# Optimization experiments

Hardware: AMD Instinct MI355X
Metric: run time of the kernel (lower is better)

Reference implementation:

```python
import jax, jax.numpy as jnp
import numpy as np


def setup_inputs() -> dict:
    key = jax.random.key(0)
    N, M, D = 4, 8192, 64
    x = jax.random.normal(key, (N, M, D), dtype=jnp.float32)
    return {"x": x, "k": 16}


def reference(x, k):
    """KNNGraph forward (algorithm='bruteforce-blas', dist='euclidean',
    exclude_self=False). Returns (src, dst) edge arrays: for each node j in
    point set i (global id i*M + j), its k nearest neighbors (including
    itself) are edge sources, the node is the destination."""
    N, M, D = x.shape
    # Squared euclidean pairwise distances via BLAS: |a|^2 + |b|^2 - 2 a.b
    x2 = jnp.sum(x * x, axis=-1)                       # (N, M)
    dots = jnp.einsum('nmd,npd->nmp', x, x)            # (N, M, M)
    d2 = x2[:, :, None] + x2[:, None, :] - 2.0 * dots  # (N, M, M)
    # k smallest distances per row -> top_k on negated distances
    _, idx = jax.lax.top_k(-d2, k)                     # (N, M, k) neighbor ids
    offset = (jnp.arange(N, dtype=idx.dtype) * M)[:, None, None]
    src = (idx + offset).reshape(-1)                   # (N*M*k,)
    dst = jnp.repeat(jnp.arange(N * M, dtype=idx.dtype), k)
    return src, dst
```

## Files before the change

### kernel.cpp

```cpp
#include <hip/hip_runtime.h>


#define MM 8192
#define NN 4
#define DD 64
#define KK 16
#define TK 20
#define TILE 64
#define NROWS (NN * MM)
#define FB 10

typedef float f32x2 __attribute__((ext_vector_type(2)));

__global__ __launch_bounds__(256) void norms_np_kernel(
    const float* __restrict__ x, float* __restrict__ x2) {
#pragma clang fp contract(off)
  int r = blockIdx.x * 256 + threadIdx.x;
  if (r >= NROWS) return;
  const float4* p = (const float4*)(x + (size_t)r * DD);
  float s[DD];
#pragma unroll
  for (int i = 0; i < DD / 4; ++i) {
    float4 v = p[i];
    s[4 * i + 0] = v.x * v.x;
    s[4 * i + 1] = v.y * v.y;
    s[4 * i + 2] = v.z * v.z;
    s[4 * i + 3] = v.w * v.w;
  }
  float acc[4][4];
#pragma unroll
  for (int c = 0; c < 4; ++c)
#pragma unroll
    for (int l = 0; l < 4; ++l) acc[c][l] = s[4 * c + l];
#pragma unroll
  for (int b = 1; b < 4; ++b)
#pragma unroll
    for (int c = 0; c < 4; ++c)
#pragma unroll
      for (int l = 0; l < 4; ++l)
        acc[c][l] = acc[c][l] + s[16 * b + 4 * c + l];
  float S[4];
#pragma unroll
  for (int l = 0; l < 4; ++l)
    S[l] = (acc[0][l] + acc[1][l]) + (acc[2][l] + acc[3][l]);
  x2[r] = (S[0] + S[1]) + (S[2] + S[3]);
}

#define PSTEP(sA, sB)                       \
  do {                                      \
    unsigned lo_ = min((sA), (sB));         \
    unsigned hi_ = max((sA), (sB));         \
    (sA) = lo_; (sB) = hi_;                 \
  } while (0)

#define PBUBBLE20(S)                                              \
  do {                                                            \
    PSTEP(S##18, S##19); PSTEP(S##17, S##18); PSTEP(S##16, S##17);\
    PSTEP(S##15, S##16); PSTEP(S##14, S##15); PSTEP(S##13, S##14);\
    PSTEP(S##12, S##13); PSTEP(S##11, S##12); PSTEP(S##10, S##11);\
    PSTEP(S##9,  S##10); PSTEP(S##8,  S##9);  PSTEP(S##7,  S##8); \
    PSTEP(S##6,  S##7);  PSTEP(S##5,  S##6);  PSTEP(S##4,  S##5); \
    PSTEP(S##3,  S##4);  PSTEP(S##2,  S##3);  PSTEP(S##1,  S##2); \
    PSTEP(S##0,  S##1);                                           \
  } while (0)

#define PDECL20(S)                                                          \
  unsigned S##0 = 0xFFFFFFFFu, S##1 = 0xFFFFFFFFu, S##2 = 0xFFFFFFFFu,      \
           S##3 = 0xFFFFFFFFu, S##4 = 0xFFFFFFFFu, S##5 = 0xFFFFFFFFu,      \
           S##6 = 0xFFFFFFFFu, S##7 = 0xFFFFFFFFu, S##8 = 0xFFFFFFFFu,      \
           S##9 = 0xFFFFFFFFu, S##10 = 0xFFFFFFFFu, S##11 = 0xFFFFFFFFu,    \
           S##12 = 0xFFFFFFFFu, S##13 = 0xFFFFFFFFu, S##14 = 0xFFFFFFFFu,   \
           S##15 = 0xFFFFFFFFu, S##16 = 0xFFFFFFFFu, S##17 = 0xFFFFFFFFu,   \
           S##18 = 0xFFFFFFFFu, S##19 = 0xFFFFFFFFu;

#define PSTORE20RAW(BASE, S)                                                \
  do {                                                                      \
    pi[(BASE) + 0]  = (int)S##0;  pi[(BASE) + 1]  = (int)S##1;              \
    pi[(BASE) + 2]  = (int)S##2;  pi[(BASE) + 3]  = (int)S##3;              \
    pi[(BASE) + 4]  = (int)S##4;  pi[(BASE) + 5]  = (int)S##5;              \
    pi[(BASE) + 6]  = (int)S##6;  pi[(BASE) + 7]  = (int)S##7;              \
    pi[(BASE) + 8]  = (int)S##8;  pi[(BASE) + 9]  = (int)S##9;              \
    pi[(BASE) + 10] = (int)S##10; pi[(BASE) + 11] = (int)S##11;             \
    pi[(BASE) + 12] = (int)S##12; pi[(BASE) + 13] = (int)S##13;             \
    pi[(BASE) + 14] = (int)S##14; pi[(BASE) + 15] = (int)S##15;             \
    pi[(BASE) + 16] = (int)S##16; pi[(BASE) + 17] = (int)S##17;             \
    pi[(BASE) + 18] = (int)S##18; pi[(BASE) + 19] = (int)S##19;             \
  } while (0)

#define PSTORE20(BASE, S, C0)                                               \
  do {                                                                      \
    pi[(BASE) + 0]  = (int)(S##0  & IMASK) + (C0);                          \
    pi[(BASE) + 1]  = (int)(S##1  & IMASK) + (C0);                          \
    pi[(BASE) + 2]  = (int)(S##2  & IMASK) + (C0);                          \
    pi[(BASE) + 3]  = (int)(S##3  & IMASK) + (C0);                          \
    pi[(BASE) + 4]  = (int)(S##4  & IMASK) + (C0);                          \
    pi[(BASE) + 5]  = (int)(S##5  & IMASK) + (C0);                          \
    pi[(BASE) + 6]  = (int)(S##6  & IMASK) + (C0);                          \
    pi[(BASE) + 7]  = (int)(S##7  & IMASK) + (C0);                          \
    pi[(BASE) + 8]  = (int)(S##8  & IMASK) + (C0);                          \
    pi[(BASE) + 9]  = (int)(S##9  & IMASK) + (C0);                          \
    pi[(BASE) + 10] = (int)(S##10 & IMASK) + (C0);                          \
    pi[(BASE) + 11] = (int)(S##11 & IMASK) + (C0);                          \
    pi[(BASE) + 12] = (int)(S##12 & IMASK) + (C0);                          \
    pi[(BASE) + 13] = (int)(S##13 & IMASK) + (C0);                          \
    pi[(BASE) + 14] = (int)(S##14 & IMASK) + (C0);                          \
    pi[(BASE) + 15] = (int)(S##15 & IMASK) + (C0);                          \
    pi[(BASE) + 16] = (int)(S##16 & IMASK) + (C0);                          \
    pi[(BASE) + 17] = (int)(S##17 & IMASK) + (C0);                          \
    pi[(BASE) + 18] = (int)(S##18 & IMASK) + (C0);                          \
    pi[(BASE) + 19] = (int)(S##19 & IMASK) + (C0);                          \
  } while (0)

#define PK2(QF4, WLO, WHI, ACC0, ACC1)                             \
  do {                                                             \
    f32x2 qlo_ = {(QF4).x, (QF4).y};                               \
    f32x2 qhi_ = {(QF4).z, (QF4).w};                               \
    ACC0 = __builtin_elementwise_fma(qlo_, (WLO), ACC0);           \
    ACC1 = __builtin_elementwise_fma(qhi_, (WHI), ACC1);           \
  } while (0)

template <int P>
__global__ __launch_bounds__(256)
__attribute__((amdgpu_waves_per_eu(2, 4)))
void knn_partial2_kernel(
    const float* __restrict__ x, const float* __restrict__ x2,
    int* __restrict__ pi) {
  constexpr int IB = (P == 16) ? 9 : (P == 8) ? 10 : (P == 4) ? 11 : 12;
  constexpr unsigned IMASK = (1u << IB) - 1u;
  constexpr unsigned QMASK = ~IMASK;

  __shared__ unsigned lbufA[FB * 256];
  __shared__ unsigned lbufB[FB * 256];

  const int tid      = threadIdx.x;
  const int rb       = blockIdx.x / P;
  const int chunk    = blockIdx.x % P;
  const int base_row = rb * 512;
  const int b        = base_row >> 13;
  const int rowA     = base_row + tid;
  const int rowB     = rowA + 256;
  const int jA       = rowA & (MM - 1);
  const int jB       = jA + 256;

  const float* __restrict__ xb  = x + (size_t)b * MM * DD;
  const float* __restrict__ x2b = x2 + b * MM;

  const float4* qpA = (const float4*)(xb + (size_t)jA * DD);
  const float4* qpB = (const float4*)(xb + (size_t)jB * DD);
  float4 qa0 = qpA[0],  qa1 = qpA[1],  qa2 = qpA[2],  qa3 = qpA[3];
  float4 qa4 = qpA[4],  qa5 = qpA[5],  qa6 = qpA[6],  qa7 = qpA[7];
  float4 qa8 = qpA[8],  qa9 = qpA[9],  qa10 = qpA[10], qa11 = qpA[11];
  float4 qa12 = qpA[12], qa13 = qpA[13], qa14 = qpA[14], qa15 = qpA[15];
  float4 qb0 = qpB[0],  qb1 = qpB[1],  qb2 = qpB[2],  qb3 = qpB[3];
  float4 qb4 = qpB[4],  qb5 = qpB[5],  qb6 = qpB[6],  qb7 = qpB[7];
  float4 qb8 = qpB[8],  qb9 = qpB[9],  qb10 = qpB[10], qb11 = qpB[11];
  float4 qb12 = qpB[12], qb13 = qpB[13], qb14 = qpB[14], qb15 = qpB[15];

  PDECL20(sa)
  PDECL20(sb)
  int cA = 0, cB = 0;

#define FLUSHQ()                                                   \
  do {                                                             \
    _Pragma("unroll")                                              \
    for (int t_ = 0; t_ < FB; ++t_) {                              \
      if (t_ < cA) {                                               \
        unsigned pk_ = lbufA[t_ * 256 + tid];                      \
        sa19 = min(sa19, pk_);                                     \
        PBUBBLE20(sa);                                             \
      }                                                            \
      if (t_ < cB) {                                               \
        unsigned pk_ = lbufB[t_ * 256 + tid];                      \
        sb19 = min(sb19, pk_);                                     \
        PBUBBLE20(sb);                                             \
      }                                                            \
    }                                                              \
    cA = 0;                                                        \
    cB = 0;                                                        \
  } while (0)

  const int C  = MM / P;
  const int c0 = chunk * C;

#pragma unroll 1
  for (int c = c0; c < c0 + C; c += 2) {
    const float4* cp0 = (const float4*)(xb + (size_t)c * DD);
    const float4* cp1 = (const float4*)(xb + (size_t)(c + 1) * DD);
    float x2c0 = x2b[c];
    float x2c1 = x2b[c + 1];

    float4 u0 = cp0[0],  u1 = cp0[1],  u2 = cp0[2],  u3 = cp0[3];
    float4 u4 = cp0[4],  u5 = cp0[5],  u6 = cp0[6],  u7 = cp0[7];
    float4 u8 = cp0[8],  u9 = cp0[9],  u10 = cp0[10], u11 = cp0[11];
    float4 u12 = cp0[12], u13 = cp0[13], u14 = cp0[14], u15 = cp0[15];
    float4 t0 = cp1[0],  t1 = cp1[1],  t2 = cp1[2],  t3 = cp1[3];
    float4 t4 = cp1[4],  t5 = cp1[5],  t6 = cp1[6],  t7 = cp1[7];
    float4 t8 = cp1[8],  t9 = cp1[9],  t10 = cp1[10], t11 = cp1[11];
    float4 t12 = cp1[12], t13 = cp1[13], t14 = cp1[14], t15 = cp1[15];

    {
      f32x2 aA0 = {0.f, 0.f}, aA1 = {0.f, 0.f};
      f32x2 aB0 = {0.f, 0.f}, aB1 = {0.f, 0.f};
      {
        f32x2 wlo, whi;
#define USEW(W)  wlo = (f32x2){(W).x, (W).y}; whi = (f32x2){(W).z, (W).w}
        USEW(u0);  PK2(qa0,  wlo, whi, aA0, aA1); PK2(qb0,  wlo, whi, aB0, aB1);
        USEW(u1);  PK2(qa1,  wlo, whi, aA0, aA1); PK2(qb1,  wlo, whi, aB0, aB1);
        USEW(u2);  PK2(qa2,  wlo, whi, aA0, aA1); PK2(qb2,  wlo, whi, aB0, aB1);
        USEW(u3);  PK2(qa3,  wlo, whi, aA0, aA1); PK2(qb3,  wlo, whi, aB0, aB1);
        USEW(u4);  PK2(qa4,  wlo, whi, aA0, aA1); PK2(qb4,  wlo, whi, aB0, aB1);
        USEW(u5);  PK2(qa5,  wlo, whi, aA0, aA1); PK2(qb5,  wlo, whi, aB0, aB1);
        USEW(u6);  PK2(qa6,  wlo, whi, aA0, aA1); PK2(qb6,  wlo, whi, aB0, aB1);
        USEW(u7);  PK2(qa7,  wlo, whi, aA0, aA1); PK2(qb7,  wlo, whi, aB0, aB1);
        USEW(u8);  PK2(qa8,  wlo, whi, aA0, aA1); PK2(qb8,  wlo, whi, aB0, aB1);
        USEW(u9);  PK2(qa9,  wlo, whi, aA0, aA1); PK2(qb9,  wlo, whi, aB0, aB1);
        USEW(u10); PK2(qa10, wlo, whi, aA0, aA1); PK2(qb10, wlo, whi, aB0, aB1);
        USEW(u11); PK2(qa11, wlo, whi, aA0, aA1); PK2(qb11, wlo, whi, aB0, aB1);
        USEW(u12); PK2(qa12, wlo, whi, aA0, aA1); PK2(qb12, wlo, whi, aB0, aB1);
        USEW(u13); PK2(qa13, wlo, whi, aA0, aA1); PK2(qb13, wlo, whi, aB0, aB1);
        USEW(u14); PK2(qa14, wlo, whi, aA0, aA1); PK2(qb14, wlo, whi, aB0, aB1);
        USEW(u15); PK2(qa15, wlo, whi, aA0, aA1); PK2(qb15, wlo, whi, aB0, aB1);
      }
      f32x2 rA = aA0 + aA1;
      f32x2 rB = aB0 + aB1;
      float dotA = rA.x + rA.y;
      float dotB = rB.x + rB.y;
      float keyA = fmaf(-2.f, dotA, x2c0);
      float keyB = fmaf(-2.f, dotB, x2c0);

      int kiA = __float_as_int(keyA);
      unsigned monoA = (unsigned)kiA ^ ((unsigned)(kiA >> 31) | 0x80000000u);
      unsigned pkA = (monoA & QMASK) | (unsigned)(c - c0);
      if (pkA < sa19) { lbufA[cA * 256 + tid] = pkA; ++cA; }

      int kiB = __float_as_int(keyB);
      unsigned monoB = (unsigned)kiB ^ ((unsigned)(kiB >> 31) | 0x80000000u);
      unsigned pkB = (monoB & QMASK) | (unsigned)(c - c0);
      if (pkB < sb19) { lbufB[cB * 256 + tid] = pkB; ++cB; }
    }

    {
      f32x2 aA0 = {0.f, 0.f}, aA1 = {0.f, 0.f};
      f32x2 aB0 = {0.f, 0.f}, aB1 = {0.f, 0.f};
      {
        f32x2 wlo, whi;
        USEW(t0);  PK2(qa0,  wlo, whi, aA0, aA1); PK2(qb0,  wlo, whi, aB0, aB1);
        USEW(t1);  PK2(qa1,  wlo, whi, aA0, aA1); PK2(qb1,  wlo, whi, aB0, aB1);
        USEW(t2);  PK2(qa2,  wlo, whi, aA0, aA1); PK2(qb2,  wlo, whi, aB0, aB1);
        USEW(t3);  PK2(qa3,  wlo, whi, aA0, aA1); PK2(qb3,  wlo, whi, aB0, aB1);
        USEW(t4);  PK2(qa4,  wlo, whi, aA0, aA1); PK2(qb4,  wlo, whi, aB0, aB1);
        USEW(t5);  PK2(qa5,  wlo, whi, aA0, aA1); PK2(qb5,  wlo, whi, aB0, aB1);
        USEW(t6);  PK2(qa6,  wlo, whi, aA0, aA1); PK2(qb6,  wlo, whi, aB0, aB1);
        USEW(t7);  PK2(qa7,  wlo, whi, aA0, aA1); PK2(qb7,  wlo, whi, aB0, aB1);
        USEW(t8);  PK2(qa8,  wlo, whi, aA0, aA1); PK2(qb8,  wlo, whi, aB0, aB1);
        USEW(t9);  PK2(qa9,  wlo, whi, aA0, aA1); PK2(qb9,  wlo, whi, aB0, aB1);
        USEW(t10); PK2(qa10, wlo, whi, aA0, aA1); PK2(qb10, wlo, whi, aB0, aB1);
        USEW(t11); PK2(qa11, wlo, whi, aA0, aA1); PK2(qb11, wlo, whi, aB0, aB1);
        USEW(t12); PK2(qa12, wlo, whi, aA0, aA1); PK2(qb12, wlo, whi, aB0, aB1);
        USEW(t13); PK2(qa13, wlo, whi, aA0, aA1); PK2(qb13, wlo, whi, aB0, aB1);
        USEW(t14); PK2(qa14, wlo, whi, aA0, aA1); PK2(qb14, wlo, whi, aB0, aB1);
        USEW(t15); PK2(qa15, wlo, whi, aA0, aA1); PK2(qb15, wlo, whi, aB0, aB1);
#undef USEW
      }
      f32x2 rA = aA0 + aA1;
      f32x2 rB = aB0 + aB1;
      float dotA = rA.x + rA.y;
      float dotB = rB.x + rB.y;
      float keyA = fmaf(-2.f, dotA, x2c1);
      float keyB = fmaf(-2.f, dotB, x2c1);

      int kiA = __float_as_int(keyA);
      unsigned monoA = (unsigned)kiA ^ ((unsigned)(kiA >> 31) | 0x80000000u);
      unsigned pkA = (monoA & QMASK) | (unsigned)(c + 1 - c0);
      if (pkA < sa19) { lbufA[cA * 256 + tid] = pkA; ++cA; }

      int kiB = __float_as_int(keyB);
      unsigned monoB = (unsigned)kiB ^ ((unsigned)(kiB >> 31) | 0x80000000u);
      unsigned pkB = (monoB & QMASK) | (unsigned)(c + 1 - c0);
      if (pkB < sb19) { lbufB[cB * 256 + tid] = pkB; ++cB; }
    }

    if (__any((cA | cB) >= FB - 2)) FLUSHQ();
  }

  FLUSHQ();
#undef FLUSHQ

  size_t baseA = ((size_t)rowA * P + chunk) * TK;
  size_t baseB = ((size_t)rowB * P + chunk) * TK;
  PSTORE20RAW(baseA, sa);
  PSTORE20RAW(baseB, sb);
}

template <int P>
__global__ __launch_bounds__(256)
__attribute__((amdgpu_waves_per_eu(2, 2)))
void knn_partial_q1_kernel(
    const float* __restrict__ x, const float* __restrict__ x2,
    int* __restrict__ pi) {
  constexpr int IB = (P == 8) ? 10 : (P == 4) ? 11 : (P == 2) ? 12 : 13;
  constexpr unsigned IMASK = (1u << IB) - 1u;
  constexpr unsigned QMASK = ~IMASK;

  __shared__ float tile[TILE * DD];
  __shared__ float x2t[TILE];

  const int tid   = threadIdx.x;
  const int rb    = blockIdx.x / P;
  const int chunk = blockIdx.x % P;
  const int b     = rb >> 5;
  const int row   = rb * 256 + tid;
  const int j     = row - b * MM;

  const float* __restrict__ xb  = x + (size_t)b * MM * DD;
  const float* __restrict__ x2b = x2 + b * MM;

  const float4* qp = (const float4*)(xb + (size_t)j * DD);
  float4 q0 = qp[0],  q1 = qp[1],  q2 = qp[2],  q3 = qp[3];
  float4 q4 = qp[4],  q5 = qp[5],  q6 = qp[6],  q7 = qp[7];
  float4 q8 = qp[8],  q9 = qp[9],  q10 = qp[10], q11 = qp[11];
  float4 q12 = qp[12], q13 = qp[13], q14 = qp[14], q15 = qp[15];

  PDECL20(s)

  const int C  = MM / P;
  const int c0 = chunk * C;

  for (int ts = c0; ts < c0 + C; ts += TILE) {
    __syncthreads();
    {
      const float4* gsrc = (const float4*)(xb + (size_t)ts * DD);
      float4* lds4 = (float4*)tile;
#pragma unroll
      for (int u = 0; u < 4; ++u) lds4[tid + 256 * u] = gsrc[tid + 256 * u];
      if (tid < TILE / 4)
        ((float4*)x2t)[tid] = ((const float4*)(x2b + ts))[tid];
    }
    __syncthreads();

#pragma unroll 2
    for (int t = 0; t < TILE; ++t) {
      const float4* cp = (const float4*)(tile + t * DD);
      f32x2 a0 = {0.f, 0.f}, a1 = {0.f, 0.f};
      {
        float4 w;
        f32x2 wlo, whi;
#define LOADW(I)  w = cp[I]; wlo = (f32x2){w.x, w.y}; whi = (f32x2){w.z, w.w}
        LOADW(0);  PK2(q0,  wlo, whi, a0, a1);
        LOADW(1);  PK2(q1,  wlo, whi, a0, a1);
        LOADW(2);  PK2(q2,  wlo, whi, a0, a1);
        LOADW(3);  PK2(q3,  wlo, whi, a0, a1);
        LOADW(4);  PK2(q4,  wlo, whi, a0, a1);
        LOADW(5);  PK2(q5,  wlo, whi, a0, a1);
        LOADW(6);  PK2(q6,  wlo, whi, a0, a1);
        LOADW(7);  PK2(q7,  wlo, whi, a0, a1);
        LOADW(8);  PK2(q8,  wlo, whi, a0, a1);
        LOADW(9);  PK2(q9,  wlo, whi, a0, a1);
        LOADW(10); PK2(q10, wlo, whi, a0, a1);
        LOADW(11); PK2(q11, wlo, whi, a0, a1);
        LOADW(12); PK2(q12, wlo, whi, a0, a1);
        LOADW(13); PK2(q13, wlo, whi, a0, a1);
        LOADW(14); PK2(q14, wlo, whi, a0, a1);
        LOADW(15); PK2(q15, wlo, whi, a0, a1);
#undef LOADW
      }
      f32x2 rr = a0 + a1;
      float dot = rr.x + rr.y;
      float key = fmaf(-2.f, dot, x2t[t]);

      int ki = __float_as_int(key);
      unsigned mono = (unsigned)ki ^ ((unsigned)(ki >> 31) | 0x80000000u);
      unsigned pk = (mono & QMASK) | (unsigned)(ts - c0 + t);
      s19 = min(s19, pk);
      PBUBBLE20(s);
    }
  }

  size_t base = ((size_t)row * P + chunk) * TK;
  PSTORE20(base, s, c0);
}

#define EBLK(QA, QB, QC, QD, W0, W1, W2, W3)                                  \
  do {                                                                        \
    v0 = (QA).x * (W0).x +                                                    \
         ((QB).x * (W1).x + ((QC).x * (W2).x + ((QD).x * (W3).x + v0)));      \
    v1 = (QA).y * (W0).y +                                                    \
         ((QB).y * (W1).y + ((QC).y * (W2).y + ((QD).y * (W3).y + v1)));      \
    v2 = (QA).z * (W0).z +                                                    \
         ((QB).z * (W1).z + ((QC).z * (W2).z + ((QD).z * (W3).z + v2)));      \
    v3 = (QA).w * (W0).w +                                                    \
         ((QB).w * (W1).w + ((QC).w * (W2).w + ((QD).w * (W3).w + v3)));      \
  } while (0)

#define LBSTEP(dA, iA, dB, iB)                                     \
  do {                                                             \
    bool s_ = ((dB) < (dA)) || ((dB) == (dA) && (iB) < (iA));      \
    float tl_ = s_ ? (dB) : (dA);                                  \
    float th_ = s_ ? (dA) : (dB);                                  \
    int   jl_ = s_ ? (iB) : (iA);                                  \
    int   jh_ = s_ ? (iA) : (iB);                                  \
    (dA) = tl_; (dB) = th_; (iA) = jl_; (iB) = jh_;                \
  } while (0)

#define RESCORE_ONE(C_)                                                     \
  {                                                                         \
    int c = (C_);                                                           \
    const float4* pp = (const float4*)(xb + (size_t)c * DD);                \
    float v0 = 0.f, v1 = 0.f, v2 = 0.f, v3 = 0.f;                           \
    {                                                                       \
      float4 w0 = pp[0], w1 = pp[1], w2 = pp[2], w3 = pp[3];                \
      EBLK(q0, q1, q2, q3, w0, w1, w2, w3);                                 \
    }                                                                       \
    {                                                                       \
      float4 w0 = pp[4], w1 = pp[5], w2 = pp[6], w3 = pp[7];                \
      EBLK(q4, q5, q6, q7, w0, w1, w2, w3);                                 \
    }                                                                       \
    {                                                                       \
      float4 w0 = pp[8], w1 = pp[9], w2 = pp[10], w3 = pp[11];              \
      EBLK(q8, q9, q10, q11, w0, w1, w2, w3);                               \
    }                                                                       \
    {                                                                       \
      float4 w0 = pp[12], w1 = pp[13], w2 = pp[14], w3 = pp[15];            \
      EBLK(q12, q13, q14, q15, w0, w1, w2, w3);                             \
    }                                                                       \
    float dotf = (v0 + v1) + (v2 + v3);                                     \
    float s  = x2j + x2[b * MM + c];                                        \
    float tm = 2.0f * dotf;                                                 \
    float d2 = s - tm;                                                      \
    bool lt = (d2 < e15) || (d2 == e15 && c < n15);                         \
    e15 = lt ? d2 : e15;                                                    \
    n15 = lt ? c : n15;                                                     \
    LBSTEP(e14, n14, e15, n15); LBSTEP(e13, n13, e14, n14);                 \
    LBSTEP(e12, n12, e13, n13); LBSTEP(e11, n11, e12, n12);                 \
    LBSTEP(e10, n10, e11, n11); LBSTEP(e9,  n9,  e10, n10);                 \
    LBSTEP(e8,  n8,  e9,  n9);  LBSTEP(e7,  n7,  e8,  n8);                  \
    LBSTEP(e6,  n6,  e7,  n7);  LBSTEP(e5,  n5,  e6,  n6);                  \
    LBSTEP(e4,  n4,  e5,  n5);  LBSTEP(e3,  n3,  e4,  n4);                  \
    LBSTEP(e2,  n2,  e3,  n3);  LBSTEP(e1,  n1,  e2,  n2);                  \
    LBSTEP(e0,  n0,  e1,  n1);                                              \
  }

#define PUBLISH_AND_MERGE8()                                                \
  {                                                                         \
    ls[sub][0][lane]  = make_uint2(MONO(e0),  (unsigned)n0);                \
    ls[sub][1][lane]  = make_uint2(MONO(e1),  (unsigned)n1);                \
    ls[sub][2][lane]  = make_uint2(MONO(e2),  (unsigned)n2);                \
    ls[sub][3][lane]  = make_uint2(MONO(e3),  (unsigned)n3);                \
    ls[sub][4][lane]  = make_uint2(MONO(e4),  (unsigned)n4);                \
    ls[sub][5][lane]  = make_uint2(MONO(e5),  (unsigned)n5);                \
    ls[sub][6][lane]  = make_uint2(MONO(e6),  (unsigned)n6);                \
    ls[sub][7][lane]  = make_uint2(MONO(e7),  (unsigned)n7);                \
    ls[sub][8][lane]  = make_uint2(MONO(e8),  (unsigned)n8);                \
    ls[sub][9][lane]  = make_uint2(MONO(e9),  (unsigned)n9);                \
    ls[sub][10][lane] = make_uint2(MONO(e10), (unsigned)n10);               \
    ls[sub][11][lane] = make_uint2(MONO(e11), (unsigned)n11);               \
    ls[sub][12][lane] = make_uint2(MONO(e12), (unsigned)n12);               \
    ls[sub][13][lane] = make_uint2(MONO(e13), (unsigned)n13);               \
    ls[sub][14][lane] = make_uint2(MONO(e14), (unsigned)n14);               \
    ls[sub][15][lane] = make_uint2(MONO(e15), (unsigned)n15);               \
    __syncthreads();                                                        \
    if (sub == 0) {                                                         \
      uint2 c0v = ls[0][0][lane], c1v = ls[1][0][lane];                     \
      uint2 c2v = ls[2][0][lane], c3v = ls[3][0][lane];                     \
      uint2 c4v = ls[4][0][lane], c5v = ls[5][0][lane];                     \
      uint2 c6v = ls[6][0][lane], c7v = ls[7][0][lane];                     \
      int h0 = 1, h1 = 1, h2 = 1, h3 = 1, h4 = 1, h5 = 1, h6 = 1, h7 = 1;   \
      const uint2 SENT = make_uint2(0xFFFFFFFFu, 0x7FFFFFFFu);              \
      for (int out = 0; out < KK; ++out) {                                  \
        bool l01 = LESS2(c0v, c1v);                                         \
        uint2 m01 = l01 ? c0v : c1v; int w01 = l01 ? 0 : 1;                 \
        bool l23 = LESS2(c2v, c3v);                                         \
        uint2 m23 = l23 ? c2v : c3v; int w23 = l23 ? 2 : 3;                 \
        bool l45 = LESS2(c4v, c5v);                                         \
        uint2 m45 = l45 ? c4v : c5v; int w45 = l45 ? 4 : 5;                 \
        bool l67 = LESS2(c6v, c7v);                                         \
        uint2 m67 = l67 ? c6v : c7v; int w67 = l67 ? 6 : 7;                 \
        bool la = LESS2(m01, m23);                                          \
        uint2 ma = la ? m01 : m23; int wa = la ? w01 : w23;                 \
        bool lb = LESS2(m45, m67);                                          \
        uint2 mb = lb ? m45 : m67; int wb = lb ? w45 : w67;                 \
        bool lf = LESS2(ma, mb);                                            \
        uint2 mv = lf ? ma : mb; int wf = lf ? wa : wb;                     \
        src[(size_t)r * KK + out] = b * MM + (int)mv.y;                     \
        dst[(size_t)r * KK + out] = r;                                      \
        if (wf == 0)      { c0v = (h0 < 16) ? ls[0][h0][lane] : SENT; ++h0; }\
        else if (wf == 1) { c1v = (h1 < 16) ? ls[1][h1][lane] : SENT; ++h1; }\
        else if (wf == 2) { c2v = (h2 < 16) ? ls[2][h2][lane] : SENT; ++h2; }\
        else if (wf == 3) { c3v = (h3 < 16) ? ls[3][h3][lane] : SENT; ++h3; }\
        else if (wf == 4) { c4v = (h4 < 16) ? ls[4][h4][lane] : SENT; ++h4; }\
        else if (wf == 5) { c5v = (h5 < 16) ? ls[5][h5][lane] : SENT; ++h5; }\
        else if (wf == 6) { c6v = (h6 < 16) ? ls[6][h6][lane] : SENT; ++h6; }\
        else              { c7v = (h7 < 16) ? ls[7][h7][lane] : SENT; ++h7; }\
      }                                                                     \
    }                                                                       \
  }

#define MONO(F) ({ int k_ = __float_as_int(F); \
                   (unsigned)k_ ^ ((unsigned)(k_ >> 31) | 0x80000000u); })
#define LESS2(A, B) ((A).x < (B).x || ((A).x == (B).x && (A).y < (B).y))

template <int P>
__global__ __launch_bounds__(256) void knn_rescore8f_kernel(
    const float* __restrict__ x, const float* __restrict__ x2,
    const int* __restrict__ pi,
    int* __restrict__ src, int* __restrict__ dst) {
#pragma clang fp contract(off)
  constexpr int IB = (P == 8) ? 10 : 11;
  constexpr unsigned IMASK = (1u << IB) - 1u;
  constexpr unsigned QMASK = ~IMASK;
  constexpr int CAND = P * TK;
  constexpr int LPT  = CAND / 8;
  constexpr int CC   = MM / P;

  __shared__ unsigned lk[8][LPT][32];
  __shared__ uint2 ls[8][16][32];
  __shared__ unsigned thr[32];

  const int tid  = threadIdx.x;
  const int lane = tid & 31;
  const int sub  = tid >> 5;
  const int r    = blockIdx.x * 32 + lane;
  const int b    = r >> 13;
  const int j    = r & (MM - 1);
  const float* __restrict__ xb = x + (size_t)b * MM * DD;
  const float x2j = x2[r];

  const float4* qp = (const float4*)(xb + (size_t)j * DD);
  float4 q0 = qp[0],  q1 = qp[1],  q2 = qp[2],  q3 = qp[3];
  float4 q4 = qp[4],  q5 = qp[5],  q6 = qp[6],  q7 = qp[7];
  float4 q8 = qp[8],  q9 = qp[9],  q10 = qp[10], q11 = qp[11];
  float4 q12 = qp[12], q13 = qp[13], q14 = qp[14], q15 = qp[15];

  {
    const uint2* pp2 =
        (const uint2*)((const unsigned*)pi + (size_t)r * CAND + sub * LPT);
#pragma unroll
    for (int i = 0; i < LPT / 2; ++i) {
      uint2 v = pp2[i];
      lk[sub][2 * i][lane]     = v.x;
      lk[sub][2 * i + 1][lane] = v.y;
    }
  }
  __syncthreads();

  if (sub == 0) {
    unsigned c0v = lk[0][0][lane], c1v = lk[1][0][lane];
    unsigned c2v = lk[2][0][lane], c3v = lk[3][0][lane];
    unsigned c4v = lk[4][0][lane], c5v = lk[5][0][lane];
    unsigned c6v = lk[6][0][lane], c7v = lk[7][0][lane];
    int h0 = 1, h1 = 1, h2 = 1, h3 = 1, h4 = 1, h5 = 1, h6 = 1, h7 = 1;
    unsigned P16 = 0;
#pragma unroll 1
    for (int out = 0; out < 16; ++out) {
      bool l01 = c0v < c1v; unsigned m01 = l01 ? c0v : c1v; int w01 = l01 ? 0 : 1;
      bool l23 = c2v < c3v; unsigned m23 = l23 ? c2v : c3v; int w23 = l23 ? 2 : 3;
      bool l45 = c4v < c5v; unsigned m45 = l45 ? c4v : c5v; int w45 = l45 ? 4 : 5;
      bool l67 = c6v < c7v; unsigned m67 = l67 ? c6v : c7v; int w67 = l67 ? 6 : 7;
      bool la = m01 < m23; unsigned ma = la ? m01 : m23; int wa = la ? w01 : w23;
      bool lb = m45 < m67; unsigned mb = lb ? m45 : m67; int wb = lb ? w45 : w67;
      bool lf = ma < mb; unsigned mv = lf ? ma : mb; int wf = lf ? wa : wb;
      P16 = mv;
      if (wf == 0)      { c0v = (h0 < LPT) ? lk[0][h0][lane] : 0xFFFFFFFFu; ++h0; }
      else if (wf == 1) { c1v = (h1 < LPT) ? lk[1][h1][lane] : 0xFFFFFFFFu; ++h1; }
      else if (wf == 2) { c2v = (h2 < LPT) ? lk[2][h2][lane] : 0xFFFFFFFFu; ++h2; }
      else if (wf == 3) { c3v = (h3 < LPT) ? lk[3][h3][lane] : 0xFFFFFFFFu; ++h3; }
      else if (wf == 4) { c4v = (h4 < LPT) ? lk[4][h4][lane] : 0xFFFFFFFFu; ++h4; }
      else if (wf == 5) { c5v = (h5 < LPT) ? lk[5][h5][lane] : 0xFFFFFFFFu; ++h5; }
      else if (wf == 6) { c6v = (h6 < LPT) ? lk[6][h6][lane] : 0xFFFFFFFFu; ++h6; }
      else              { c7v = (h7 < LPT) ? lk[7][h7][lane] : 0xFFFFFFFFu; ++h7; }
    }
    thr[lane] = ((P16 & QMASK) + (1u << IB)) | IMASK;
  }
  __syncthreads();
  const unsigned T = thr[lane];

  const float INF = __builtin_inff();
  float e0 = INF, e1 = INF, e2 = INF, e3 = INF, e4 = INF, e5 = INF,
        e6 = INF, e7 = INF, e8 = INF, e9 = INF, e10 = INF, e11 = INF,
        e12 = INF, e13 = INF, e14 = INF, e15 = INF;
  int n0 = 0x7fffffff, n1 = 0x7fffffff, n2 = 0x7fffffff, n3 = 0x7fffffff,
      n4 = 0x7fffffff, n5 = 0x7fffffff, n6 = 0x7fffffff, n7 = 0x7fffffff,
      n8 = 0x7fffffff, n9 = 0x7fffffff, n10 = 0x7fffffff, n11 = 0x7fffffff,
      n12 = 0x7fffffff, n13 = 0x7fffffff, n14 = 0x7fffffff, n15 = 0x7fffffff;

#pragma unroll 1
  for (int t = 0; t < LPT; ++t) {
    unsigned pk = lk[sub][t][lane];
    if (__all((int)(pk > T))) break;
    if (pk <= T) {
      int ent = sub * LPT + t;
      int chunk = ent / TK;
      RESCORE_ONE((int)(pk & IMASK) + chunk * CC)
    }
  }

  PUBLISH_AND_MERGE8()
}

__global__ __launch_bounds__(256) void knn_rescore16f_kernel(
    const float* __restrict__ x, const float* __restrict__ x2,
    const int* __restrict__ pi,
    int* __restrict__ src, int* __restrict__ dst) {
#pragma clang fp contract(off)
  constexpr int IB = 9;
  constexpr unsigned IMASK = (1u << IB) - 1u;
  constexpr unsigned QMASK = ~IMASK;
  constexpr int CAND = 16 * TK;
  constexpr int LPT  = CAND / 8;
  constexpr int CC   = MM / 16;

  __shared__ unsigned lk[16][TK][32];
  __shared__ uint2 ls[8][16][32];
  __shared__ unsigned thr[32];

  const int tid  = threadIdx.x;
  const int lane = tid & 31;
  const int sub  = tid >> 5;
  const int r    = blockIdx.x * 32 + lane;
  const int b    = r >> 13;
  const int j    = r & (MM - 1);
  const float* __restrict__ xb = x + (size_t)b * MM * DD;
  const float x2j = x2[r];

  const float4* qp = (const float4*)(xb + (size_t)j * DD);
  float4 q0 = qp[0],  q1 = qp[1],  q2 = qp[2],  q3 = qp[3];
  float4 q4 = qp[4],  q5 = qp[5],  q6 = qp[6],  q7 = qp[7];
  float4 q8 = qp[8],  q9 = qp[9],  q10 = qp[10], q11 = qp[11];
  float4 q12 = qp[12], q13 = qp[13], q14 = qp[14], q15 = qp[15];

  {
    const uint2* pp2 =
        (const uint2*)((const unsigned*)pi + (size_t)r * CAND + sub * LPT);
#pragma unroll
    for (int i = 0; i < LPT / 2; ++i) {
      int e = sub * LPT + 2 * i;
      uint2 v = pp2[i];
      lk[e / TK][e % TK][lane]       = v.x;
      lk[e / TK][e % TK + 1][lane]   = v.y;
    }
  }
  __syncthreads();

  if (sub == 0) {
    unsigned d0 = lk[0][0][lane],  d1 = lk[1][0][lane];
    unsigned d2 = lk[2][0][lane],  d3 = lk[3][0][lane];
    unsigned d4 = lk[4][0][lane],  d5 = lk[5][0][lane];
    unsigned d6 = lk[6][0][lane],  d7 = lk[7][0][lane];
    unsigned d8 = lk[8][0][lane],  d9 = lk[9][0][lane];
    unsigned d10 = lk[10][0][lane], d11 = lk[11][0][lane];
    unsigned d12 = lk[12][0][lane], d13 = lk[13][0][lane];
    unsigned d14 = lk[14][0][lane], d15 = lk[15][0][lane];
    int g0 = 1, g1 = 1, g2 = 1, g3 = 1, g4 = 1, g5 = 1, g6 = 1, g7 = 1;
    int g8 = 1, g9 = 1, g10 = 1, g11 = 1, g12 = 1, g13 = 1, g14 = 1, g15 = 1;
    unsigned P16 = 0;
#pragma unroll 1
    for (int out = 0; out < 16; ++out) {
      bool lA = d0 < d1;   unsigned mA = lA ? d0 : d1;   int wA = lA ? 0 : 1;
      bool lB = d2 < d3;   unsigned mB = lB ? d2 : d3;   int wB = lB ? 2 : 3;
      bool lC = d4 < d5;   unsigned mC = lC ? d4 : d5;   int wC = lC ? 4 : 5;
      bool lD = d6 < d7;   unsigned mD = lD ? d6 : d7;   int wD = lD ? 6 : 7;
      bool lE = d8 < d9;   unsigned mE = lE ? d8 : d9;   int wE = lE ? 8 : 9;
      bool lF = d10 < d11; unsigned mF = lF ? d10 : d11; int wF = lF ? 10 : 11;
      bool lG = d12 < d13; unsigned mG = lG ? d12 : d13; int wG = lG ? 12 : 13;
      bool lH = d14 < d15; unsigned mH = lH ? d14 : d15; int wH = lH ? 14 : 15;
      bool lI = mA < mB; unsigned mI = lI ? mA : mB; int wI = lI ? wA : wB;
      bool lJ = mC < mD; unsigned mJ = lJ ? mC : mD; int wJ = lJ ? wC : wD;
      bool lK = mE < mF; unsigned mK = lK ? mE : mF; int wK = lK ? wE : wF;
      bool lL = mG < mH; unsigned mL = lL ? mG : mH; int wL = lL ? wG : wH;
      bool lM = mI < mJ; unsigned mM = lM ? mI : mJ; int wM = lM ? wI : wJ;
      bool lN = mK < mL; unsigned mN = lN ? mK : mL; int wN = lN ? wK : wL;
      bool lZ = mM < mN; unsigned mv = lZ ? mM : mN; int wf = lZ ? wM : wN;
      P16 = mv;
      if (wf == 0)       { d0  = (g0  < TK) ? lk[0][g0][lane]   : 0xFFFFFFFFu; ++g0; }
      else if (wf == 1)  { d1  = (g1  < TK) ? lk[1][g1][lane]   : 0xFFFFFFFFu; ++g1; }
      else if (wf == 2)  { d2  = (g2  < TK) ? lk[2][g2][lane]   : 0xFFFFFFFFu; ++g2; }
      else if (wf == 3)  { d3  = (g3  < TK) ? lk[3][g3][lane]   : 0xFFFFFFFFu; ++g3; }
      else if (wf == 4)  { d4  = (g4  < TK) ? lk[4][g4][lane]   : 0xFFFFFFFFu; ++g4; }
      else if (wf == 5)  { d5  = (g5  < TK) ? lk[5][g5][lane]   : 0xFFFFFFFFu; ++g5; }
      else if (wf == 6)  { d6  = (g6  < TK) ? lk[6][g6][lane]   : 0xFFFFFFFFu; ++g6; }
      else if (wf == 7)  { d7  = (g7  < TK) ? lk[7][g7][lane]   : 0xFFFFFFFFu; ++g7; }
      else if (wf == 8)  { d8  = (g8  < TK) ? lk[8][g8][lane]   : 0xFFFFFFFFu; ++g8; }
      else if (wf == 9)  { d9  = (g9  < TK) ? lk[9][g9][lane]   : 0xFFFFFFFFu; ++g9; }
      else if (wf == 10) { d10 = (g10 < TK) ? lk[10][g10][lane] : 0xFFFFFFFFu; ++g10; }
      else if (wf == 11) { d11 = (g11 < TK) ? lk[11][g11][lane] : 0xFFFFFFFFu; ++g11; }
      else if (wf == 12) { d12 = (g12 < TK) ? lk[12][g12][lane] : 0xFFFFFFFFu; ++g12; }
      else if (wf == 13) { d13 = (g13 < TK) ? lk[13][g13][lane] : 0xFFFFFFFFu; ++g13; }
      else if (wf == 14) { d14 = (g14 < TK) ? lk[14][g14][lane] : 0xFFFFFFFFu; ++g14; }
      else               { d15 = (g15 < TK) ? lk[15][g15][lane] : 0xFFFFFFFFu; ++g15; }
    }
    thr[lane] = ((P16 & QMASK) + (1u << IB)) | IMASK;
  }
  __syncthreads();
  const unsigned T = thr[lane];

  const float INF = __builtin_inff();
  float e0 = INF, e1 = INF, e2 = INF, e3 = INF, e4 = INF, e5 = INF,
        e6 = INF, e7 = INF, e8 = INF, e9 = INF, e10 = INF, e11 = INF,
        e12 = INF, e13 = INF, e14 = INF, e15 = INF;
  int n0 = 0x7fffffff, n1 = 0x7fffffff, n2 = 0x7fffffff, n3 = 0x7fffffff,
      n4 = 0x7fffffff, n5 = 0x7fffffff, n6 = 0x7fffffff, n7 = 0x7fffffff,
      n8 = 0x7fffffff, n9 = 0x7fffffff, n10 = 0x7fffffff, n11 = 0x7fffffff,
      n12 = 0x7fffffff, n13 = 0x7fffffff, n14 = 0x7fffffff, n15 = 0x7fffffff;

#pragma unroll 1
  for (int cs = 0; cs < 2; ++cs) {
    const int ch = 2 * sub + cs;
#pragma unroll 1
    for (int t = 0; t < TK; ++t) {
      unsigned pk = lk[ch][t][lane];
      if (__all((int)(pk > T))) break;
      if (pk <= T) {
        RESCORE_ONE((int)(pk & IMASK) + ch * CC)
      }
    }
  }

  PUBLISH_AND_MERGE8()
}

template <int P>
__global__ __launch_bounds__(256) void knn_rescore8_kernel(
    const float* __restrict__ x, const float* __restrict__ x2,
    const int* __restrict__ pi,
    int* __restrict__ src, int* __restrict__ dst) {
#pragma clang fp contract(off)
  constexpr int CAND = P * TK;
  constexpr int LPT  = CAND / 8;
  __shared__ uint2 ls[8][16][32];

  const int tid  = threadIdx.x;
  const int lane = tid & 31;
  const int sub  = tid >> 5;
  const int r    = blockIdx.x * 32 + lane;
  const int b    = r >> 13;
  const int j    = r & (MM - 1);
  const float* __restrict__ xb = x + (size_t)b * MM * DD;
  const float x2j = x2[r];

  const float4* qp = (const float4*)(xb + (size_t)j * DD);
  float4 q0 = qp[0],  q1 = qp[1],  q2 = qp[2],  q3 = qp[3];
  float4 q4 = qp[4],  q5 = qp[5],  q6 = qp[6],  q7 = qp[7];
  float4 q8 = qp[8],  q9 = qp[9],  q10 = qp[10], q11 = qp[11];
  float4 q12 = qp[12], q13 = qp[13], q14 = qp[14], q15 = qp[15];

  const float INF = __builtin_inff();
  float e0 = INF, e1 = INF, e2 = INF, e3 = INF, e4 = INF, e5 = INF,
        e6 = INF, e7 = INF, e8 = INF, e9 = INF, e10 = INF, e11 = INF,
        e12 = INF, e13 = INF, e14 = INF, e15 = INF;
  int n0 = 0x7fffffff, n1 = 0x7fffffff, n2 = 0x7fffffff, n3 = 0x7fffffff,
      n4 = 0x7fffffff, n5 = 0x7fffffff, n6 = 0x7fffffff, n7 = 0x7fffffff,
      n8 = 0x7fffffff, n9 = 0x7fffffff, n10 = 0x7fffffff, n11 = 0x7fffffff,
      n12 = 0x7fffffff, n13 = 0x7fffffff, n14 = 0x7fffffff, n15 = 0x7fffffff;

  size_t base = (size_t)r * CAND + (size_t)sub * LPT;

  for (int t = 0; t < LPT; ++t) {
    RESCORE_ONE(pi[base + t])
  }

  PUBLISH_AND_MERGE8()
}

extern "C" void kernel_launch(void* const* d_in, const int* in_sizes, int n_in,
                              void* d_out, int out_size, void* d_ws, size_t ws_size,
                              hipStream_t stream) {
  const float* x = (const float*)d_in[0];
  int* out = (int*)d_out;

  char* ws = (char*)d_ws;
  float* x2 = (float*)ws;
  int*   pi = (int*)(ws + (size_t)NROWS * sizeof(float));
  int* src = out;
  int* dst = out + (size_t)NROWS * KK;

  auto need = [](int P) {
    return (size_t)NROWS * sizeof(float) +
           (size_t)NROWS * P * TK * sizeof(int);
  };

  norms_np_kernel<<<NROWS / 256, 256, 0, stream>>>(x, x2);

  if (ws_size >= need(16)) {
    knn_partial2_kernel<16><<<(NROWS / 512) * 16, 256, 0, stream>>>(x, x2, pi);
    knn_rescore16f_kernel<<<NROWS / 32, 256, 0, stream>>>(x, x2, pi, src, dst);
  } else if (ws_size >= need(8)) {
    knn_partial2_kernel<8><<<(NROWS / 512) * 8, 256, 0, stream>>>(x, x2, pi);
    knn_rescore8f_kernel<8><<<NROWS / 32, 256, 0, stream>>>(x, x2, pi, src, dst);
  } else if (ws_size >= need(4)) {
    knn_partial2_kernel<4><<<(NROWS / 512) * 4, 256, 0, stream>>>(x, x2, pi);
    knn_rescore8f_kernel<4><<<NROWS / 32, 256, 0, stream>>>(x, x2, pi, src, dst);
  } else if (ws_size >= need(2)) {
    knn_partial_q1_kernel<2><<<(NROWS / 256) * 2, 256, 0, stream>>>(x, x2, pi);
    knn_rescore8_kernel<2><<<NROWS / 32, 256, 0, stream>>>(x, x2, pi, src, dst);
  } else {
    knn_partial_q1_kernel<1><<<(NROWS / 256) * 1, 256, 0, stream>>>(x, x2, pi);
    knn_rescore8_kernel<1><<<NROWS / 32, 256, 0, stream>>>(x, x2, pi, src, dst);
  }
}
```

Before: 708.7 us.

## Drop 16-way column split path and pin partial kernel to one wave per EU

Removes the P=16 partial/rescore path so the default dispatch uses the 8-way column split with the rescore8f kernel, halving candidate count and workspace traffic per row but giving fewer blocks in the partial pass. Also changes the partial kernel's waves-per-EU hint from (2,4) to (1,1), letting the compiler use more registers at the cost of occupancy and latency hiding.

```diff
diff --git a/kernel.cpp b/kernel.cpp
--- a/kernel.cpp
+++ b/kernel.cpp
@@ -121,11 +121,11 @@
 
 template <int P>
 __global__ __launch_bounds__(256)
-__attribute__((amdgpu_waves_per_eu(2, 4)))
+__attribute__((amdgpu_waves_per_eu(1, 1)))
 void knn_partial2_kernel(
     const float* __restrict__ x, const float* __restrict__ x2,
     int* __restrict__ pi) {
-  constexpr int IB = (P == 16) ? 9 : (P == 8) ? 10 : (P == 4) ? 11 : 12;
+  constexpr int IB = (P == 8) ? 10 : (P == 4) ? 11 : 12;
   constexpr unsigned IMASK = (1u << IB) - 1u;
   constexpr unsigned QMASK = ~IMASK;
 
@@ -597,127 +597,6 @@
   PUBLISH_AND_MERGE8()
 }
 
-__global__ __launch_bounds__(256) void knn_rescore16f_kernel(
-    const float* __restrict__ x, const float* __restrict__ x2,
-    const int* __restrict__ pi,
-    int* __restrict__ src, int* __restrict__ dst) {
-#pragma clang fp contract(off)
-  constexpr int IB = 9;
-  constexpr unsigned IMASK = (1u << IB) - 1u;
-  constexpr unsigned QMASK = ~IMASK;
-  constexpr int CAND = 16 * TK;
-  constexpr int LPT  = CAND / 8;
-  constexpr int CC   = MM / 16;
-
-  __shared__ unsigned lk[16][TK][32];
-  __shared__ uint2 ls[8][16][32];
-  __shared__ unsigned thr[32];
-
-  const int tid  = threadIdx.x;
-  const int lane = tid & 31;
-  const int sub  = tid >> 5;
-  const int r    = blockIdx.x * 32 + lane;
-  const int b    = r >> 13;
-  const int j    = r & (MM - 1);
-  const float* __restrict__ xb = x + (size_t)b * MM * DD;
-  const float x2j = x2[r];
-
-  const float4* qp = (const float4*)(xb + (size_t)j * DD);
-  float4 q0 = qp[0],  q1 = qp[1],  q2 = qp[2],  q3 = qp[3];
-  float4 q4 = qp[4],  q5 = qp[5],  q6 = qp[6],  q7 = qp[7];
-  float4 q8 = qp[8],  q9 = qp[9],  q10 = qp[10], q11 = qp[11];
-  float4 q12 = qp[12], q13 = qp[13], q14 = qp[14], q15 = qp[15];
-
-  {
-    const uint2* pp2 =
-        (const uint2*)((const unsigned*)pi + (size_t)r * CAND + sub * LPT);
-#pragma unroll
-    for (int i = 0; i < LPT / 2; ++i) {
-      int e = sub * LPT + 2 * i;
-      uint2 v = pp2[i];
-      lk[e / TK][e % TK][lane]       = v.x;
-      lk[e / TK][e % TK + 1][lane]   = v.y;
-    }
-  }
-  __syncthreads();
-
-  if (sub == 0) {
-    unsigned d0 = lk[0][0][lane],  d1 = lk[1][0][lane];
-    unsigned d2 = lk[2][0][lane],  d3 = lk[3][0][lane];
-    unsigned d4 = lk[4][0][lane],  d5 = lk[5][0][lane];
-    unsigned d6 = lk[6][0][lane],  d7 = lk[7][0][lane];
-    unsigned d8 = lk[8][0][lane],  d9 = lk[9][0][lane];
-    unsigned d10 = lk[10][0][lane], d11 = lk[11][0][lane];
-    unsigned d12 = lk[12][0][lane], d13 = lk[13][0][lane];
-    unsigned d14 = lk[14][0][lane], d15 = lk[15][0][lane];
-    int g0 = 1, g1 = 1, g2 = 1, g3 = 1, g4 = 1, g5 = 1, g6 = 1, g7 = 1;
-    int g8 = 1, g9 = 1, g10 = 1, g11 = 1, g12 = 1, g13 = 1, g14 = 1, g15 = 1;
-    unsigned P16 = 0;
-#pragma unroll 1
-    for (int out = 0; out < 16; ++out) {
-      bool lA = d0 < d1;   unsigned mA = lA ? d0 : d1;   int wA = lA ? 0 : 1;
-      bool lB = d2 < d3;   unsigned mB = lB ? d2 : d3;   int wB = lB ? 2 : 3;
-      bool lC = d4 < d5;   unsigned mC = lC ? d4 : d5;   int wC = lC ? 4 : 5;
-      bool lD = d6 < d7;   unsigned mD = lD ? d6 : d7;   int wD = lD ? 6 : 7;
-      bool lE = d8 < d9;   unsigned mE = lE ? d8 : d9;   int wE = lE ? 8 : 9;
-      bool lF = d10 < d11; unsigned mF = lF ? d10 : d11; int wF = lF ? 10 : 11;
-      bool lG = d12 < d13; unsigned mG = lG ? d12 : d13; int wG = lG ? 12 : 13;
-      bool lH = d14 < d15; unsigned mH = lH ? d14 : d15; int wH = lH ? 14 : 15;
-      bool lI = mA < mB; unsigned mI = lI ? mA : mB; int wI = lI ? wA : wB;
-      bool lJ = mC < mD; unsigned mJ = lJ ? mC : mD; int wJ = lJ ? wC : wD;
-      bool lK = mE < mF; unsigned mK = lK ? mE : mF; int wK = lK ? wE : wF;
-      bool lL = mG < mH; unsigned mL = lL ? mG : mH; int wL = lL ? wG : wH;
-      bool lM = mI < mJ; unsigned mM = lM ? mI : mJ; int wM = lM ? wI : wJ;
-      bool lN = mK < mL; unsigned mN = lN ? mK : mL; int wN = lN ? wK : wL;
-      bool lZ = mM < mN; unsigned mv = lZ ? mM : mN; int wf = lZ ? wM : wN;
-      P16 = mv;
-      if (wf == 0)       { d0  = (g0  < TK) ? lk[0][g0][lane]   : 0xFFFFFFFFu; ++g0; }
-      else if (wf == 1)  { d1  = (g1  < TK) ? lk[1][g1][lane]   : 0xFFFFFFFFu; ++g1; }
-      else if (wf == 2)  { d2  = (g2  < TK) ? lk[2][g2][lane]   : 0xFFFFFFFFu; ++g2; }
-      else if (wf == 3)  { d3  = (g3  < TK) ? lk[3][g3][lane]   : 0xFFFFFFFFu; ++g3; }
-      else if (wf == 4)  { d4  = (g4  < TK) ? lk[4][g4][lane]   : 0xFFFFFFFFu; ++g4; }
-      else if (wf == 5)  { d5  = (g5  < TK) ? lk[5][g5][lane]   : 0xFFFFFFFFu; ++g5; }
-      else if (wf == 6)  { d6  = (g6  < TK) ? lk[6][g6][lane]   : 0xFFFFFFFFu; ++g6; }
-      else if (wf == 7)  { d7  = (g7  < TK) ? lk[7][g7][lane]   : 0xFFFFFFFFu; ++g7; }
-      else if (wf == 8)  { d8  = (g8  < TK) ? lk[8][g8][lane]   : 0xFFFFFFFFu; ++g8; }
-      else if (wf == 9)  { d9  = (g9  < TK) ? lk[9][g9][lane]   : 0xFFFFFFFFu; ++g9; }
-      else if (wf == 10) { d10 = (g10 < TK) ? lk[10][g10][lane] : 0xFFFFFFFFu; ++g10; }
-      else if (wf == 11) { d11 = (g11 < TK) ? lk[11][g11][lane] : 0xFFFFFFFFu; ++g11; }
-      else if (wf == 12) { d12 = (g12 < TK) ? lk[12][g12][lane] : 0xFFFFFFFFu; ++g12; }
-      else if (wf == 13) { d13 = (g13 < TK) ? lk[13][g13][lane] : 0xFFFFFFFFu; ++g13; }
-      else if (wf == 14) { d14 = (g14 < TK) ? lk[14][g14][lane] : 0xFFFFFFFFu; ++g14; }
-      else               { d15 = (g15 < TK) ? lk[15][g15][lane] : 0xFFFFFFFFu; ++g15; }
-    }
-    thr[lane] = ((P16 & QMASK) + (1u << IB)) | IMASK;
-  }
-  __syncthreads();
-  const unsigned T = thr[lane];
-
-  const float INF = __builtin_inff();
-  float e0 = INF, e1 = INF, e2 = INF, e3 = INF, e4 = INF, e5 = INF,
-        e6 = INF, e7 = INF, e8 = INF, e9 = INF, e10 = INF, e11 = INF,
-        e12 = INF, e13 = INF, e14 = INF, e15 = INF;
-  int n0 = 0x7fffffff, n1 = 0x7fffffff, n2 = 0x7fffffff, n3 = 0x7fffffff,
-      n4 = 0x7fffffff, n5 = 0x7fffffff, n6 = 0x7fffffff, n7 = 0x7fffffff,
-      n8 = 0x7fffffff, n9 = 0x7fffffff, n10 = 0x7fffffff, n11 = 0x7fffffff,
-      n12 = 0x7fffffff, n13 = 0x7fffffff, n14 = 0x7fffffff, n15 = 0x7fffffff;
-
-#pragma unroll 1
-  for (int cs = 0; cs < 2; ++cs) {
-    const int ch = 2 * sub + cs;
-#pragma unroll 1
-    for (int t = 0; t < TK; ++t) {
-      unsigned pk = lk[ch][t][lane];
-      if (__all((int)(pk > T))) break;
-      if (pk <= T) {
-        RESCORE_ONE((int)(pk & IMASK) + ch * CC)
-      }
-    }
-  }
-
-  PUBLISH_AND_MERGE8()
-}
-
 template <int P>
 __global__ __launch_bounds__(256) void knn_rescore8_kernel(
     const float* __restrict__ x, const float* __restrict__ x2,
@@ -780,10 +659,7 @@
 
   norms_np_kernel<<<NROWS / 256, 256, 0, stream>>>(x, x2);
 
-  if (ws_size >= need(16)) {
-    knn_partial2_kernel<16><<<(NROWS / 512) * 16, 256, 0, stream>>>(x, x2, pi);
-    knn_rescore16f_kernel<<<NROWS / 32, 256, 0, stream>>>(x, x2, pi, src, dst);
-  } else if (ws_size >= need(8)) {
+  if (ws_size >= need(8)) {
     knn_partial2_kernel<8><<<(NROWS / 512) * 8, 256, 0, stream>>>(x, x2, pi);
     knn_rescore8f_kernel<8><<<NROWS / 32, 256, 0, stream>>>(x, x2, pi, src, dst);
   } else if (ws_size >= need(4)) {
```

Result: slower. 916.0 us (+29.2%).
